# Kernel tuning notes

Measured on AMD Instinct MI355X. Metric: run time of the kernel, lower is better.

The kernel has to match this reference:

```python
import jax, jax.numpy as jnp
import numpy as np

G = 100000   # num graphs
N = 2000000  # num nodes
E = 4000000  # num edges (unused downstream, kept for fidelity)
D = 300      # emb_dim
L = 50       # num noise levels


def setup_inputs() -> dict:
    key = jax.random.key(0)
    ks = jax.random.split(key, 12)
    node2graph = jnp.sort(jax.random.randint(ks[0], (N,), 0, G))
    edge_index = jax.random.randint(ks[1], (2, E), 0, N)
    noise_level = jax.random.randint(ks[2], (G,), 0, L)
    molecule_repr = jax.random.normal(ks[3], (G, D), dtype=jnp.float32)
    pos_noise_pred = jax.random.normal(ks[4], (N, 3), dtype=jnp.float32)
    pos_perturbed = jax.random.normal(ks[5], (N, 3), dtype=jnp.float32)
    pos_target = jax.random.normal(ks[6], (N, 3), dtype=jnp.float32)
    s = 1.0 / np.sqrt(D)
    W1 = jax.random.uniform(ks[7], (D, D), minval=-s, maxval=s, dtype=jnp.float32)
    b1 = jax.random.uniform(ks[8], (D,), minval=-s, maxval=s, dtype=jnp.float32)
    W2 = jax.random.uniform(ks[9], (D, D), minval=-s, maxval=s, dtype=jnp.float32)
    b2 = jax.random.uniform(ks[10], (D,), minval=-s, maxval=s, dtype=jnp.float32)
    sigmas = jnp.asarray(np.exp(np.linspace(np.log(10.0), np.log(0.01), L)), dtype=jnp.float32)
    return dict(node2graph=node2graph, edge_index=edge_index, noise_level=noise_level,
                num_graphs=G, molecule_repr=molecule_repr, pos_noise_pred=pos_noise_pred,
                pos_perturbed=pos_perturbed, pos_target=pos_target,
                W1=W1, b1=b1, W2=W2, b2=b2, sigmas=sigmas)


def _score_target_riemann(pos_perturbed, pos_target, node2graph, num_graphs):
    # @torch.no_grad() branch: all scatter_mean/scatter_add indexed by node2graph
    seg_sum = lambda x: jax.ops.segment_sum(x, node2graph, num_segments=num_graphs)
    cnt = jnp.maximum(seg_sum(jnp.ones((node2graph.shape[0],), jnp.float32)), 1.0)[:, None]
    center = seg_sum(pos_target) / cnt                 # [G,3]
    p_center = seg_sum(pos_perturbed) / cnt            # [G,3]
    pos_c = pos_target - center[node2graph]            # [N,3]
    pp_c = pos_perturbed - p_center[node2graph]        # [N,3]
    # per-graph 3x3 matrices: ptp[i,j] = sum pp_i*pp_j, otp[i,j] = sum pos_c_i*pp_j
    ptp = seg_sum(pp_c[:, :, None] * pp_c[:, None, :])   # [G,3,3]
    otp = seg_sum(pos_c[:, :, None] * pp_c[:, None, :])  # [G,3,3]
    ptp_n = ptp[node2graph]                              # [N,3,3]
    otp_n = otp[node2graph]                              # [N,3,3]
    num = -2.0 * (jnp.einsum('ni,nij->nj', pp_c, ptp_n)
                  - jnp.einsum('ni,nij->nj', pos_c, otp_n))  # [N,3]
    den = (jnp.linalg.norm(ptp_n.reshape(-1, 9), axis=-1)
           + jnp.linalg.norm(otp_n.reshape(-1, 9), axis=-1))[:, None]
    return num / den


def reference(node2graph, edge_index, noise_level, num_graphs, molecule_repr,
              pos_noise_pred, pos_perturbed, pos_target, W1, b1, W2, b2, sigmas):
    edge2graph = node2graph[edge_index[0]]  # computed but unused, as in original
    used_sigmas = sigmas[noise_level][node2graph][:, None]  # [N,1]
    score_target = jax.lax.stop_gradient(
        _score_target_riemann(pos_perturbed, pos_target, node2graph, num_graphs)
    ) / used_sigmas
    pred_noise = (pos_noise_pred - pos_perturbed) * (1.0 / used_sigmas)
    per_node = jnp.sum((pred_noise - score_target) ** 2, axis=-1)  # [N]
    per_graph = jax.ops.segment_sum(per_node, node2graph, num_segments=num_graphs)
    pos_denoise = per_graph.mean()
    # noise-level prediction head: Linear -> SiLU -> Linear, CE over noise_level
    h = jax.nn.silu(molecule_repr @ W1 + b1)
    logits = h @ W2 + b2  # [G,D]
    logp = jax.nn.log_softmax(logits, axis=-1)
    ce = -jnp.take_along_axis(logp, noise_level[:, None], axis=1)[:, 0]
    loss_pred_noise = ce.mean()
    return jnp.stack([pos_denoise, loss_pred_noise])
```

## Files before the change

### kernel.cpp

```cpp
#include <hip/hip_runtime.h>
#include <math.h>


typedef __attribute__((ext_vector_type(8))) short bf16x8;
typedef __attribute__((ext_vector_type(4))) short s16x4;
typedef __attribute__((ext_vector_type(4))) float f32x4;

__device__ __forceinline__ short bt(float f) {
    return (short)(__float_as_uint(f) >> 16);
}

#define TM   64
#define DRL  300
#define DP   320
#define XS   328
#define NT   20
#define MT   4
#define KCH  10


__device__ __forceinline__ void prod22(const float* A, const float* B, int j,
                                       float* dst) {
    float a0 = A[3*j], a1 = A[3*j+1], a2 = A[3*j+2];
    float b0 = B[3*j], b1 = B[3*j+1], b2 = B[3*j+2];
    dst[0] = 1.f;
    dst[1] = a0;  dst[2] = a1;  dst[3] = a2;
    dst[4] = b0;  dst[5] = b1;  dst[6] = b2;
    dst[7] = b0*b0;  dst[8] = b0*b1;  dst[9] = b0*b2;
    dst[10] = b1*b1; dst[11] = b1*b2; dst[12] = b2*b2;
    dst[13] = a0*b0; dst[14] = a0*b1; dst[15] = a0*b2;
    dst[16] = a1*b0; dst[17] = a1*b1; dst[18] = a1*b2;
    dst[19] = a2*b0; dst[20] = a2*b1; dst[21] = a2*b2;
}

__device__ __forceinline__ void acc22(float* q, const float* A, const float* B,
                                      int j) {
    float p[22];
    prod22(A, B, j, p);
#pragma unroll
    for (int k = 0; k < 22; ++k) q[k] += p[k];
}

__device__ __forceinline__ void flush_store(float* __restrict__ mom, int seg,
                                            const float* v) {
    float4* d = (float4*)&mom[seg * 24];
    float4 s0 = {v[0], v[1], v[2], v[3]};
    float4 s1 = {v[4], v[5], v[6], v[7]};
    float4 s2 = {v[8], v[9], v[10], v[11]};
    float4 s3 = {v[12], v[13], v[14], v[15]};
    float4 s4 = {v[16], v[17], v[18], v[19]};
    float4 s5 = {v[20], v[21], 0.f, 0.f};
    d[0] = s0; d[1] = s1; d[2] = s2; d[3] = s3; d[4] = s4; d[5] = s5;
}

__device__ __forceinline__ void flush_atomic(float* __restrict__ mom, int seg,
                                             const float* v) {
    float* m = &mom[seg * 24];
#pragma unroll
    for (int k = 0; k < 22; ++k) atomicAdd(&m[k], v[k]);
}

__global__ __launch_bounds__(256)
void k_moments(const int* __restrict__ n2g,
               const float* __restrict__ pt,
               const float* __restrict__ pp,
               float* __restrict__ mom, int N) {
    const int t = blockIdx.x * blockDim.x + threadIdx.x;
    const int lane = threadIdx.x & 63;
    const int i0 = t * 4;
    const bool act = (i0 < N);

    float A[12], B[12];
    int g0 = -1, g1 = -1, g2 = -1, g3 = -1;
    if (act) {
        const float4* ptv = (const float4*)pt;
        const float4* ppv = (const float4*)pp;
#pragma unroll
        for (int v = 0; v < 3; ++v) {
            float4 x = ptv[3 * t + v];
            A[4*v+0] = x.x; A[4*v+1] = x.y; A[4*v+2] = x.z; A[4*v+3] = x.w;
            float4 y = ppv[3 * t + v];
            B[4*v+0] = y.x; B[4*v+1] = y.y; B[4*v+2] = y.z; B[4*v+3] = y.w;
        }
        int4 gv = *(const int4*)&n2g[i0];
        g0 = gv.x; g1 = gv.y; g2 = gv.z; g3 = gv.w;
    }

    float q[22];
    float lead[22];
    int curseg = g0, leadseg = -2;
    bool haveLead = false;
#pragma unroll
    for (int k = 0; k < 22; ++k) { q[k] = 0.f; lead[k] = 0.f; }
    if (act) {
        prod22(A, B, 0, q);
        const int gj[3] = {g1, g2, g3};
#pragma unroll
        for (int j = 1; j < 4; ++j) {
            int gg = gj[j - 1];
            if (gg == curseg) {
                acc22(q, A, B, j);
            } else {
                if (!haveLead) {
                    haveLead = true; leadseg = curseg;
#pragma unroll
                    for (int k = 0; k < 22; ++k) lead[k] = q[k];
                } else {
                    flush_store(mom, curseg, q);
                }
                prod22(A, B, j, q);
                curseg = gg;
            }
        }
    }

    const int waveFirstNode = ((t - lane) & 0x7FFFFFFF) * 4;
    int before_seg = -1, after_seg = -1;
    if (lane == 0 && waveFirstNode > 0 && waveFirstNode <= N)
        before_seg = n2g[waveFirstNode - 1];
    before_seg = __shfl(before_seg, 0, 64);
    const int waveLast = waveFirstNode + 255;
    if (lane == 63 && waveLast + 1 < N) after_seg = n2g[waveLast + 1];
    after_seg = __shfl(after_seg, 63, 64);

#pragma unroll
    for (int d = 1; d < 64; d <<= 1) {
        int ps = __shfl_up(curseg, d, 64);
        bool ok = (lane >= d) && (ps == curseg);
#pragma unroll
        for (int k = 0; k < 22; ++k) {
            float o = __shfl_up(q[k], d, 64);
            q[k] += ok ? o : 0.f;
        }
    }

    int pseg = __shfl_up(curseg, 1, 64);
    bool cont = act && haveLead && (lane > 0) && (pseg == leadseg);
    float pcnt = 0.f;
#pragma unroll
    for (int k = 0; k < 22; ++k) {
        float pv = __shfl_up(q[k], 1, 64);
        if (k == 0) pcnt = pv;
        lead[k] += cont ? pv : 0.f;
    }
    if (act && haveLead) {
        bool covers = (lane == 0) || (cont && (pcnt == (float)(lane * 4)));
        bool ileft = covers && (before_seg == leadseg);
        if (ileft) flush_atomic(mom, leadseg, lead);
        else       flush_store(mom, leadseg, lead);
    }

    int nseg0 = __shfl_down(g0, 1, 64);
    bool tail = act && ((lane == 63) || (nseg0 != curseg));
    if (tail) {
        bool covers = (q[0] == (float)(lane * 4 + 4));
        bool ileft = covers && (before_seg == curseg);
        bool iright = (lane == 63) && (after_seg == curseg);
        if (ileft || iright) flush_atomic(mom, curseg, q);
        else                 flush_store(mom, curseg, q);
    }
}

__global__ void k_node(const int* __restrict__ n2g,
                       const float* __restrict__ pt,
                       const float* __restrict__ pp,
                       const float* __restrict__ pnp,
                       const float* __restrict__ mom,
                       const int* __restrict__ nl,
                       const float* __restrict__ sigmas,
                       double* __restrict__ accA, int N) {
    int t = blockIdx.x * blockDim.x + threadIdx.x;
    int i0 = t * 4;
    float q = 0.f;
    if (i0 < N) {
        float A[12], B[12], C[12];
        const float4* ptv = (const float4*)pt;
        const float4* ppv = (const float4*)pp;
        const float4* pnv = (const float4*)pnp;
#pragma unroll
        for (int v = 0; v < 3; ++v) {
            float4 x = ptv[3 * t + v];
            A[4*v+0] = x.x; A[4*v+1] = x.y; A[4*v+2] = x.z; A[4*v+3] = x.w;
            float4 y = ppv[3 * t + v];
            B[4*v+0] = y.x; B[4*v+1] = y.y; B[4*v+2] = y.z; B[4*v+3] = y.w;
            float4 z = pnv[3 * t + v];
            C[4*v+0] = z.x; C[4*v+1] = z.y; C[4*v+2] = z.z; C[4*v+3] = z.w;
        }
        int4 gv = *(const int4*)&n2g[i0];
        int gl[4] = {gv.x, gv.y, gv.z, gv.w};
        int gcur = -1;
        float c0=0,c1=0,c2=0,d0=0,d1=0,d2=0,p00=0,p01=0,p02=0,p11=0,p12=0,p22=0;
        float o00=0,o01=0,o02=0,o10=0,o11=0,o12=0,o20=0,o21=0,o22=0,idn=0,is2=0;
#pragma unroll
        for (int j = 0; j < 4; ++j) {
            int i = i0 + j;
            if (i >= N) break;
            int g = gl[j];
            if (g != gcur) {
                gcur = g;
                const float4* pr = (const float4*)&mom[g * 24];
                float4 v0 = pr[0], v1 = pr[1], v2 = pr[2],
                       v3 = pr[3], v4 = pr[4], v5 = pr[5];
                float cnt = fmaxf(v0.x, 1.f);
                float ic = 1.f / cnt;
                c0 = v0.y * ic; c1 = v0.z * ic; c2 = v0.w * ic;
                d0 = v1.x * ic; d1 = v1.y * ic; d2 = v1.z * ic;
                p00 = v1.w - cnt*d0*d0; p01 = v2.x - cnt*d0*d1;
                p02 = v2.y - cnt*d0*d2; p11 = v2.z - cnt*d1*d1;
                p12 = v2.w - cnt*d1*d2; p22 = v3.x - cnt*d2*d2;
                o00 = v3.y - cnt*c0*d0; o01 = v3.z - cnt*c0*d1;
                o02 = v3.w - cnt*c0*d2; o10 = v4.x - cnt*c1*d0;
                o11 = v4.y - cnt*c1*d1; o12 = v4.z - cnt*c1*d2;
                o20 = v4.w - cnt*c2*d0; o21 = v5.x - cnt*c2*d1;
                o22 = v5.y - cnt*c2*d2;
                float ptn = sqrtf(p00*p00 + p11*p11 + p22*p22 +
                                  2.f*(p01*p01 + p02*p02 + p12*p12));
                float otn = sqrtf(o00*o00 + o01*o01 + o02*o02 +
                                  o10*o10 + o11*o11 + o12*o12 +
                                  o20*o20 + o21*o21 + o22*o22);
                float den = ptn + otn;
                idn = (den > 0.f) ? (1.f / den) : 0.f;
                float sg = sigmas[nl[g]];
                is2 = 1.f / (sg * sg);
            }
            float a0 = A[3*j+0] - c0, a1 = A[3*j+1] - c1, a2 = A[3*j+2] - c2;
            float b0 = B[3*j+0] - d0, b1 = B[3*j+1] - d1, b2 = B[3*j+2] - d2;
            float n0 = -2.f * ((b0*p00 + b1*p01 + b2*p02) - (a0*o00 + a1*o10 + a2*o20));
            float n1 = -2.f * ((b0*p01 + b1*p11 + b2*p12) - (a0*o01 + a1*o11 + a2*o21));
            float n2 = -2.f * ((b0*p02 + b1*p12 + b2*p22) - (a0*o02 + a1*o12 + a2*o22));
            float e0 = (C[3*j+0] - B[3*j+0]) - n0 * idn;
            float e1 = (C[3*j+1] - B[3*j+1]) - n1 * idn;
            float e2 = (C[3*j+2] - B[3*j+2]) - n2 * idn;
            q += (e0*e0 + e1*e1 + e2*e2) * is2;
        }
    }
    for (int o = 32; o > 0; o >>= 1) q += __shfl_down(q, o, 64);
    int wv = (threadIdx.x >> 6);
    if ((threadIdx.x & 63) == 0)
        atomicAdd(&accA[(blockIdx.x * 4 + wv) & 255], (double)q);
}


__global__ void k_prepw(const float* __restrict__ W1, const float* __restrict__ W2,
                        short* __restrict__ Wb1, short* __restrict__ Wb2) {
    int id = blockIdx.x * blockDim.x + threadIdx.x;
    if (id >= 2 * DP * DP) return;
    int mat = id / (DP * DP);
    int rem = id - mat * DP * DP;
    int k = rem / DP, n = rem - (rem / DP) * DP;
    const float* W = mat ? W2 : W1;
    short* Wb = mat ? Wb2 : Wb1;
    float v = (k < DRL && n < DRL) ? W[k * DRL + n] : 0.f;
    int kc = k >> 5, kin = k & 31, quad = kin >> 3, j = kin & 7;
    int t = n >> 4, l16 = n & 15;
    Wb[(((kc * NT + t) * 64) + quad * 16 + l16) * 8 + j] = bt(v);
}


__global__ __launch_bounds__(640, 3)
void k_mlp(const float* __restrict__ X,
           const short* __restrict__ Wb1, const short* __restrict__ Wb2,
           const float* __restrict__ b1, const float* __restrict__ b2,
           const int* __restrict__ nl,
           double* __restrict__ accC, int G) {
    __shared__ __align__(16) short Xs[TM * XS];
    __shared__ __align__(16) short Hs[TM * XS];

    const int tid  = threadIdx.x;
    const int wv   = tid >> 6;
    const int lane = tid & 63;
    const int quad = lane >> 4;
    const int l16  = lane & 15;
    const int m0   = blockIdx.x * TM;

    const bf16x8* B1 = (const bf16x8*)Wb1;
    const bf16x8* B2 = (const bf16x8*)Wb2;
    const int tile0 = wv * 2, tile1 = wv * 2 + 1;

    bf16x8 w1a[KCH], w1b[KCH];
#pragma unroll
    for (int kc = 0; kc < KCH; ++kc) {
        w1a[kc] = B1[(kc * NT + tile0) * 64 + lane];
        w1b[kc] = B1[(kc * NT + tile1) * 64 + lane];
    }

    const float4* Xv = (const float4*)X;
    {
        float4 xv[8];
#pragma unroll
        for (int u = 0; u < 8; ++u) {
            int idx = tid + u * 640;
            float4 v = {0.f, 0.f, 0.f, 0.f};
            if (idx < TM * 75) {
                int r = idx / 75, c = idx - r * 75;
                int gr = m0 + r;
                if (gr < G) v = Xv[gr * 75 + c];
            }
            xv[u] = v;
        }
#pragma unroll
        for (int u = 0; u < 8; ++u) {
            int idx = tid + u * 640;
            if (idx < TM * 75) {
                int r = idx / 75, c = idx - r * 75;
                s16x4 sv = { bt(xv[u].x), bt(xv[u].y), bt(xv[u].z), bt(xv[u].w) };
                *(s16x4*)&Xs[r * XS + c * 4] = sv;
            }
        }
    }
    for (int idx = tid; idx < TM * (DP - DRL); idx += 640) {
        int r = idx / (DP - DRL), c = idx - r * (DP - DRL);
        Xs[r * XS + DRL + c] = 0;
    }
    __syncthreads();

    f32x4 acc[MT][2];
    const f32x4 vzero = {0.f, 0.f, 0.f, 0.f};
#pragma unroll
    for (int m = 0; m < MT; ++m) { acc[m][0] = vzero; acc[m][1] = vzero; }

#pragma unroll
    for (int kc = 0; kc < KCH; ++kc) {
        bf16x8 a[MT];
#pragma unroll
        for (int m = 0; m < MT; ++m)
            a[m] = *(const bf16x8*)&Xs[(m * 16 + l16) * XS + kc * 32 + quad * 8];
#pragma unroll
        for (int m = 0; m < MT; ++m) {
            acc[m][0] = __builtin_amdgcn_mfma_f32_16x16x32_bf16(a[m], w1a[kc], acc[m][0], 0, 0, 0);
            acc[m][1] = __builtin_amdgcn_mfma_f32_16x16x32_bf16(a[m], w1b[kc], acc[m][1], 0, 0, 0);
        }
    }

    bf16x8 w2a[KCH], w2b[KCH];
#pragma unroll
    for (int kc = 0; kc < KCH; ++kc) {
        w2a[kc] = B2[(kc * NT + tile0) * 64 + lane];
        w2b[kc] = B2[(kc * NT + tile1) * 64 + lane];
    }

#pragma unroll
    for (int t = 0; t < 2; ++t) {
        int col = (wv * 2 + t) * 16 + l16;
        float bias = (col < DRL) ? b1[col] : 0.f;
#pragma unroll
        for (int m = 0; m < MT; ++m)
#pragma unroll
            for (int r = 0; r < 4; ++r) {
                float v = acc[m][t][r] + bias;
                float h = v / (1.f + __expf(-v));
                Hs[(m * 16 + quad * 4 + r) * XS + col] = bt(h);
            }
    }
    __syncthreads();

#pragma unroll
    for (int m = 0; m < MT; ++m) { acc[m][0] = vzero; acc[m][1] = vzero; }
#pragma unroll
    for (int kc = 0; kc < KCH; ++kc) {
        bf16x8 a[MT];
#pragma unroll
        for (int m = 0; m < MT; ++m)
            a[m] = *(const bf16x8*)&Hs[(m * 16 + l16) * XS + kc * 32 + quad * 8];
#pragma unroll
        for (int m = 0; m < MT; ++m) {
            acc[m][0] = __builtin_amdgcn_mfma_f32_16x16x32_bf16(a[m], w2a[kc], acc[m][0], 0, 0, 0);
            acc[m][1] = __builtin_amdgcn_mfma_f32_16x16x32_bf16(a[m], w2b[kc], acc[m][1], 0, 0, 0);
        }
    }

    float* S = (float*)Xs;
    float* T = S + TM * 10;
    const int colA = tile0 * 16 + l16;
    const int colB = tile1 * 16 + l16;
    const float biasA = (colA < DRL) ? b2[colA] : 0.f;
    const float biasB = (colB < DRL) ? b2[colB] : 0.f;
#pragma unroll
    for (int m = 0; m < MT; ++m) {
#pragma unroll
        for (int r = 0; r < 4; ++r) {
            int row = m * 16 + quad * 4 + r;
            int grow = m0 + row;
            int ct = (grow < G) ? nl[grow] : -1;
            float lgA = acc[m][0][r] + biasA;
            float lgB = acc[m][1][r] + biasB;
            float sw = ((colA < DRL) ? __expf(lgA) : 0.f) +
                       ((colB < DRL) ? __expf(lgB) : 0.f);
            for (int o = 1; o < 16; o <<= 1) sw += __shfl_xor(sw, o, 64);
            if (l16 == 0) S[row * 10 + wv] = sw;
            if (colA == ct) T[row] = lgA;
            if (colB == ct) T[row] = lgB;
        }
    }
    __syncthreads();
    if (tid < 64) {
        int row = tid;
        int grow = m0 + row;
        float q = 0.f;
        if (grow < G) {
            float ss = 0.f;
#pragma unroll
            for (int w = 0; w < 10; ++w) ss += S[row * 10 + w];
            q = __logf(ss) - T[row];
        }
        for (int o = 32; o > 0; o >>= 1) q += __shfl_down(q, o, 64);
        if (tid == 0) atomicAdd(&accC[blockIdx.x & 255], (double)q);
    }
}


__global__ void k_final(const double* __restrict__ accA,
                        const double* __restrict__ accC,
                        float* __restrict__ out, float invG) {
    int t = threadIdx.x;
    double a = accA[t] + accA[t + 64] + accA[t + 128] + accA[t + 192];
    double c = accC[t] + accC[t + 64] + accC[t + 128] + accC[t + 192];
    for (int o = 32; o > 0; o >>= 1) {
        a += __shfl_down(a, o, 64);
        c += __shfl_down(c, o, 64);
    }
    if (t == 0) {
        out[0] = (float)(a * (double)invG);
        out[1] = (float)(c * (double)invG);
    }
}


extern "C" void kernel_launch(void* const* d_in, const int* in_sizes, int n_in,
                              void* d_out, int out_size, void* d_ws, size_t ws_size,
                              hipStream_t stream) {
    const int*   n2g = (const int*)d_in[0];
    const int*   nl  = (const int*)d_in[2];
    const float* X   = (const float*)d_in[4];
    const float* pnp = (const float*)d_in[5];
    const float* pp  = (const float*)d_in[6];
    const float* pt  = (const float*)d_in[7];
    const float* W1  = (const float*)d_in[8];
    const float* b1  = (const float*)d_in[9];
    const float* W2  = (const float*)d_in[10];
    const float* b2  = (const float*)d_in[11];
    const float* sig = (const float*)d_in[12];

    const int N = in_sizes[0];
    const int G = in_sizes[2];

    double* accA = (double*)d_ws;
    double* accC = accA + 256;
    short*  Wb1  = (short*)((char*)d_ws + 4096);
    short*  Wb2  = Wb1 + DP * DP;
    float*  mom  = (float*)((char*)d_ws + 4096 + (size_t)2 * DP * DP * 2);

    hipMemsetAsync(d_ws, 0, 4096, stream);
    hipMemsetAsync(mom, 0, (size_t)G * 24 * 4, stream);

    const int T4 = (N + 3) / 4;
    k_prepw<<<(2 * DP * DP + 255) / 256, 256, 0, stream>>>(W1, W2, Wb1, Wb2);
    k_moments<<<(T4 + 255) / 256, 256, 0, stream>>>(n2g, pt, pp, mom, N);
    k_node<<<(T4 + 255) / 256, 256, 0, stream>>>(n2g, pt, pp, pnp, mom,
                                                 nl, sig, accA, N);
    k_mlp<<<(G + TM - 1) / TM, 640, 0, stream>>>(X, Wb1, Wb2, b1, b2, nl,
                                                 accC, G);
    k_final<<<1, 64, 0, stream>>>(accA, accC, (float*)d_out, 1.0f / (float)G);
}
```

Before: 410.1 us.

## Make MLP kernel persistent with double-buffered X tiles and 2x5 warp tiling

Turns k_mlp into a persistent kernel with at most 256 blocks, each looping over 64-row tiles. The next tile's X rows are prefetched from global memory and written to a second LDS buffer while the current tile computes. Waves now use a 2x5 layout (32 rows by 4 column tiles each) and stream weight fragments through a 3-slot register ring instead of holding all of W1/W2 in registers. It also accumulates CE locally with one atomic per block. This reduces launch count, register pressure and exposed load latency, but 256 blocks may underfill the GPU and each wave now reloads weights from cache on every tile.

```diff
diff --git a/kernel.cpp b/kernel.cpp
--- a/kernel.cpp
+++ b/kernel.cpp
@@ -15,8 +15,8 @@
 #define DP   320
 #define XS   328
 #define NT   20
-#define MT   4
 #define KCH  10
+#define GRID_MLP 256
 
 
 __device__ __forceinline__ void prod22(const float* A, const float* B, int j,
@@ -257,155 +257,201 @@
 }
 
 
+#define MFMA8(SS)                                                              \
+    do {                                                                       \
+        _Pragma("unroll")                                                      \
+        for (int n = 0; n < 4; ++n) {                                          \
+            acc[0][n] = __builtin_amdgcn_mfma_f32_16x16x32_bf16(a0, SS[n],     \
+                                                        acc[0][n], 0, 0, 0);  \
+            acc[1][n] = __builtin_amdgcn_mfma_f32_16x16x32_bf16(a1, SS[n],     \
+                                                        acc[1][n], 0, 0, 0);  \
+        }                                                                      \
+    } while (0)
+
+__device__ __forceinline__ void mfma_gemm(const bf16x8* __restrict__ Bm,
+                                          const short* As, int wm, int tb,
+                                          int lane, int l16, int quad,
+                                          f32x4 acc[2][4]) {
+    bf16x8 s0[4], s1[4], s2[4];
+#pragma unroll
+    for (int n = 0; n < 4; ++n) s0[n] = Bm[(0 * NT + tb + n) * 64 + lane];
+#pragma unroll
+    for (int n = 0; n < 4; ++n) s1[n] = Bm[(1 * NT + tb + n) * 64 + lane];
+#pragma unroll
+    for (int kc = 0; kc < KCH; ++kc) {
+        if (kc + 2 < KCH) {
+            const int slot = (kc + 2) % 3;
+            if (slot == 0) {
+#pragma unroll
+                for (int n = 0; n < 4; ++n)
+                    s0[n] = Bm[((kc + 2) * NT + tb + n) * 64 + lane];
+            } else if (slot == 1) {
+#pragma unroll
+                for (int n = 0; n < 4; ++n)
+                    s1[n] = Bm[((kc + 2) * NT + tb + n) * 64 + lane];
+            } else {
+#pragma unroll
+                for (int n = 0; n < 4; ++n)
+                    s2[n] = Bm[((kc + 2) * NT + tb + n) * 64 + lane];
+            }
+        }
+        bf16x8 a0 = *(const bf16x8*)&As[(wm * 32 + l16) * XS + kc * 32 + quad * 8];
+        bf16x8 a1 = *(const bf16x8*)&As[(wm * 32 + 16 + l16) * XS + kc * 32 + quad * 8];
+        if (kc % 3 == 0)      MFMA8(s0);
+        else if (kc % 3 == 1) MFMA8(s1);
+        else                  MFMA8(s2);
+    }
+}
+
 __global__ __launch_bounds__(640, 3)
 void k_mlp(const float* __restrict__ X,
            const short* __restrict__ Wb1, const short* __restrict__ Wb2,
            const float* __restrict__ b1, const float* __restrict__ b2,
            const int* __restrict__ nl,
-           double* __restrict__ accC, int G) {
-    __shared__ __align__(16) short Xs[TM * XS];
+           double* __restrict__ accC, int G, int ntiles) {
+    __shared__ __align__(16) short Xs[2][TM * XS];
     __shared__ __align__(16) short Hs[TM * XS];
+    __shared__ float S[TM * 5];
+    __shared__ float T[TM];
 
     const int tid  = threadIdx.x;
     const int wv   = tid >> 6;
     const int lane = tid & 63;
     const int quad = lane >> 4;
     const int l16  = lane & 15;
-    const int m0   = blockIdx.x * TM;
+    const int wm   = wv / 5;
+    const int wn   = wv - wm * 5;
+    const int tb   = wn * 4;
 
     const bf16x8* B1 = (const bf16x8*)Wb1;
     const bf16x8* B2 = (const bf16x8*)Wb2;
-    const int tile0 = wv * 2, tile1 = wv * 2 + 1;
-
-    bf16x8 w1a[KCH], w1b[KCH];
-#pragma unroll
-    for (int kc = 0; kc < KCH; ++kc) {
-        w1a[kc] = B1[(kc * NT + tile0) * 64 + lane];
-        w1b[kc] = B1[(kc * NT + tile1) * 64 + lane];
-    }
-
     const float4* Xv = (const float4*)X;
+
+    for (int idx = tid; idx < 2 * TM * (DP - DRL); idx += 640) {
+        int b   = idx / (TM * (DP - DRL));
+        int rem = idx - b * (TM * (DP - DRL));
+        int r = rem / (DP - DRL), c = rem - r * (DP - DRL);
+        Xs[b][r * XS + DRL + c] = 0;
+    }
+
     {
-        float4 xv[8];
+        const int m0 = blockIdx.x * TM;
 #pragma unroll
         for (int u = 0; u < 8; ++u) {
             int idx = tid + u * 640;
             float4 v = {0.f, 0.f, 0.f, 0.f};
+            int r = idx / 75, c = idx - r * 75;
+            if (idx < TM * 75 && m0 + r < G) v = Xv[(m0 + r) * 75 + c];
             if (idx < TM * 75) {
+                s16x4 sv = { bt(v.x), bt(v.y), bt(v.z), bt(v.w) };
+                *(s16x4*)&Xs[0][r * XS + c * 4] = sv;
+            }
+        }
+    }
+    __syncthreads();
+
+    double ce_local = 0.0;
+    int cur = 0;
+    for (int t = blockIdx.x; t < ntiles; t += GRID_MLP) {
+        const int m0 = t * TM;
+        const int tn = t + GRID_MLP;
+        const bool hasnext = (tn < ntiles);
+
+        f32x4 acc[2][4];
+        const f32x4 vzero = {0.f, 0.f, 0.f, 0.f};
+#pragma unroll
+        for (int m = 0; m < 2; ++m)
+#pragma unroll
+            for (int n = 0; n < 4; ++n) acc[m][n] = vzero;
+        mfma_gemm(B1, &Xs[cur][0], wm, tb, lane, l16, quad, acc);
+
+        float4 xr[8];
+        if (hasnext) {
+            const int m0n = tn * TM;
+#pragma unroll
+            for (int u = 0; u < 8; ++u) {
+                int idx = tid + u * 640;
+                float4 v = {0.f, 0.f, 0.f, 0.f};
                 int r = idx / 75, c = idx - r * 75;
-                int gr = m0 + r;
-                if (gr < G) v = Xv[gr * 75 + c];
-            }
-            xv[u] = v;
-        }
-#pragma unroll
-        for (int u = 0; u < 8; ++u) {
-            int idx = tid + u * 640;
-            if (idx < TM * 75) {
-                int r = idx / 75, c = idx - r * 75;
-                s16x4 sv = { bt(xv[u].x), bt(xv[u].y), bt(xv[u].z), bt(xv[u].w) };
-                *(s16x4*)&Xs[r * XS + c * 4] = sv;
-            }
-        }
-    }
-    for (int idx = tid; idx < TM * (DP - DRL); idx += 640) {
-        int r = idx / (DP - DRL), c = idx - r * (DP - DRL);
-        Xs[r * XS + DRL + c] = 0;
-    }
-    __syncthreads();
-
-    f32x4 acc[MT][2];
-    const f32x4 vzero = {0.f, 0.f, 0.f, 0.f};
-#pragma unroll
-    for (int m = 0; m < MT; ++m) { acc[m][0] = vzero; acc[m][1] = vzero; }
-
-#pragma unroll
-    for (int kc = 0; kc < KCH; ++kc) {
-        bf16x8 a[MT];
-#pragma unroll
-        for (int m = 0; m < MT; ++m)
-            a[m] = *(const bf16x8*)&Xs[(m * 16 + l16) * XS + kc * 32 + quad * 8];
-#pragma unroll
-        for (int m = 0; m < MT; ++m) {
-            acc[m][0] = __builtin_amdgcn_mfma_f32_16x16x32_bf16(a[m], w1a[kc], acc[m][0], 0, 0, 0);
-            acc[m][1] = __builtin_amdgcn_mfma_f32_16x16x32_bf16(a[m], w1b[kc], acc[m][1], 0, 0, 0);
-        }
-    }
-
-    bf16x8 w2a[KCH], w2b[KCH];
-#pragma unroll
-    for (int kc = 0; kc < KCH; ++kc) {
-        w2a[kc] = B2[(kc * NT + tile0) * 64 + lane];
-        w2b[kc] = B2[(kc * NT + tile1) * 64 + lane];
-    }
-
-#pragma unroll
-    for (int t = 0; t < 2; ++t) {
-        int col = (wv * 2 + t) * 16 + l16;
-        float bias = (col < DRL) ? b1[col] : 0.f;
-#pragma unroll
-        for (int m = 0; m < MT; ++m)
+                if (idx < TM * 75 && m0n + r < G) v = Xv[(m0n + r) * 75 + c];
+                xr[u] = v;
+            }
+        }
+
+#pragma unroll
+        for (int nt = 0; nt < 4; ++nt) {
+            int col = (tb + nt) * 16 + l16;
+            float bias = (col < DRL) ? b1[col] : 0.f;
+#pragma unroll
+            for (int m = 0; m < 2; ++m)
+#pragma unroll
+                for (int r = 0; r < 4; ++r) {
+                    float v = acc[m][nt][r] + bias;
+                    float h = v / (1.f + __expf(-v));
+                    Hs[(wm * 32 + m * 16 + quad * 4 + r) * XS + col] = bt(h);
+                }
+        }
+
+        if (hasnext) {
+#pragma unroll
+            for (int u = 0; u < 8; ++u) {
+                int idx = tid + u * 640;
+                if (idx < TM * 75) {
+                    int r = idx / 75, c = idx - r * 75;
+                    s16x4 sv = { bt(xr[u].x), bt(xr[u].y), bt(xr[u].z), bt(xr[u].w) };
+                    *(s16x4*)&Xs[cur ^ 1][r * XS + c * 4] = sv;
+                }
+            }
+        }
+        __syncthreads();
+
+#pragma unroll
+        for (int m = 0; m < 2; ++m)
+#pragma unroll
+            for (int n = 0; n < 4; ++n) acc[m][n] = vzero;
+        mfma_gemm(B2, &Hs[0], wm, tb, lane, l16, quad, acc);
+
+        float biasB[4];
+#pragma unroll
+        for (int nt = 0; nt < 4; ++nt) {
+            int col = (tb + nt) * 16 + l16;
+            biasB[nt] = (col < DRL) ? b2[col] : 0.f;
+        }
+#pragma unroll
+        for (int m = 0; m < 2; ++m)
 #pragma unroll
             for (int r = 0; r < 4; ++r) {
-                float v = acc[m][t][r] + bias;
-                float h = v / (1.f + __expf(-v));
-                Hs[(m * 16 + quad * 4 + r) * XS + col] = bt(h);
-            }
-    }
-    __syncthreads();
-
-#pragma unroll
-    for (int m = 0; m < MT; ++m) { acc[m][0] = vzero; acc[m][1] = vzero; }
-#pragma unroll
-    for (int kc = 0; kc < KCH; ++kc) {
-        bf16x8 a[MT];
-#pragma unroll
-        for (int m = 0; m < MT; ++m)
-            a[m] = *(const bf16x8*)&Hs[(m * 16 + l16) * XS + kc * 32 + quad * 8];
-#pragma unroll
-        for (int m = 0; m < MT; ++m) {
-            acc[m][0] = __builtin_amdgcn_mfma_f32_16x16x32_bf16(a[m], w2a[kc], acc[m][0], 0, 0, 0);
-            acc[m][1] = __builtin_amdgcn_mfma_f32_16x16x32_bf16(a[m], w2b[kc], acc[m][1], 0, 0, 0);
-        }
-    }
-
-    float* S = (float*)Xs;
-    float* T = S + TM * 10;
-    const int colA = tile0 * 16 + l16;
-    const int colB = tile1 * 16 + l16;
-    const float biasA = (colA < DRL) ? b2[colA] : 0.f;
-    const float biasB = (colB < DRL) ? b2[colB] : 0.f;
-#pragma unroll
-    for (int m = 0; m < MT; ++m) {
-#pragma unroll
-        for (int r = 0; r < 4; ++r) {
-            int row = m * 16 + quad * 4 + r;
-            int grow = m0 + row;
-            int ct = (grow < G) ? nl[grow] : -1;
-            float lgA = acc[m][0][r] + biasA;
-            float lgB = acc[m][1][r] + biasB;
-            float sw = ((colA < DRL) ? __expf(lgA) : 0.f) +
-                       ((colB < DRL) ? __expf(lgB) : 0.f);
-            for (int o = 1; o < 16; o <<= 1) sw += __shfl_xor(sw, o, 64);
-            if (l16 == 0) S[row * 10 + wv] = sw;
-            if (colA == ct) T[row] = lgA;
-            if (colB == ct) T[row] = lgB;
-        }
-    }
-    __syncthreads();
-    if (tid < 64) {
-        int row = tid;
-        int grow = m0 + row;
-        float q = 0.f;
-        if (grow < G) {
-            float ss = 0.f;
-#pragma unroll
-            for (int w = 0; w < 10; ++w) ss += S[row * 10 + w];
-            q = __logf(ss) - T[row];
-        }
-        for (int o = 32; o > 0; o >>= 1) q += __shfl_down(q, o, 64);
-        if (tid == 0) atomicAdd(&accC[blockIdx.x & 255], (double)q);
-    }
+                int row  = wm * 32 + m * 16 + quad * 4 + r;
+                int grow = m0 + row;
+                int ct   = (grow < G) ? nl[grow] : -1;
+                float sw = 0.f;
+#pragma unroll
+                for (int nt = 0; nt < 4; ++nt) {
+                    int col = (tb + nt) * 16 + l16;
+                    float lg = acc[m][nt][r] + biasB[nt];
+                    if (col < DRL) sw += __expf(lg);
+                    if (col == ct) T[row] = lg;
+                }
+                for (int o = 1; o < 16; o <<= 1) sw += __shfl_xor(sw, o, 64);
+                if (l16 == 0) S[row * 5 + wn] = sw;
+            }
+        __syncthreads();
+
+        if (tid < 64) {
+            int row = tid, grow = m0 + row;
+            float q = 0.f;
+            if (grow < G) {
+                float ss = S[row*5+0] + S[row*5+1] + S[row*5+2] +
+                           S[row*5+3] + S[row*5+4];
+                q = __logf(ss) - T[row];
+            }
+            for (int o = 32; o > 0; o >>= 1) q += __shfl_down(q, o, 64);
+            if (tid == 0) ce_local += (double)q;
+        }
+        cur ^= 1;
+    }
+    if (tid == 0 && ce_local != 0.0)
+        atomicAdd(&accC[blockIdx.x & 255], ce_local);
 }
 
 
@@ -454,11 +500,14 @@
     hipMemsetAsync(mom, 0, (size_t)G * 24 * 4, stream);
 
     const int T4 = (N + 3) / 4;
+    const int ntiles = (G + TM - 1) / TM;
+    const int grid_mlp = (ntiles < GRID_MLP) ? ntiles : GRID_MLP;
+
     k_prepw<<<(2 * DP * DP + 255) / 256, 256, 0, stream>>>(W1, W2, Wb1, Wb2);
     k_moments<<<(T4 + 255) / 256, 256, 0, stream>>>(n2g, pt, pp, mom, N);
     k_node<<<(T4 + 255) / 256, 256, 0, stream>>>(n2g, pt, pp, pnp, mom,
                                                  nl, sig, accA, N);
-    k_mlp<<<(G + TM - 1) / TM, 640, 0, stream>>>(X, Wb1, Wb2, b1, b2, nl,
-                                                 accC, G);
+    k_mlp<<<grid_mlp, 640, 0, stream>>>(X, Wb1, Wb2, b1, b2, nl,
+                                        accC, G, ntiles);
     k_final<<<1, 64, 0, stream>>>(accA, accC, (float*)d_out, 1.0f / (float)G);
 }
```

New measurement: 555.6 us. 35.5% more time.
